# Optimization experiments

Hardware: AMD Instinct MI355X
Metric: run time of the kernel (lower is better)

Reference implementation:

```python
import jax, jax.numpy as jnp
import numpy as np

N_UNITS = 512
H = 8
D_K = N_UNITS // H  # 64
B = 4
T = 1024


def setup_inputs() -> dict:
    key = jax.random.key(0)
    ks = jax.random.split(key, 10)
    s = 0.02
    return {
        "x": jax.random.normal(ks[0], (B * T, N_UNITS), dtype=jnp.float32),
        "pos_k": jax.random.normal(ks[1], (T, T, D_K), dtype=jnp.float32),
        "batch_size": B,
        "Wq": jax.random.normal(ks[2], (N_UNITS, N_UNITS), dtype=jnp.float32) * s,
        "bq": jax.random.normal(ks[3], (N_UNITS,), dtype=jnp.float32) * s,
        "Wk": jax.random.normal(ks[4], (N_UNITS, N_UNITS), dtype=jnp.float32) * s,
        "bk": jax.random.normal(ks[5], (N_UNITS,), dtype=jnp.float32) * s,
        "Wv": jax.random.normal(ks[6], (N_UNITS, N_UNITS), dtype=jnp.float32) * s,
        "bv": jax.random.normal(ks[7], (N_UNITS,), dtype=jnp.float32) * s,
        "Wo": jax.random.normal(ks[8], (N_UNITS, N_UNITS), dtype=jnp.float32) * s,
        "bo": jax.random.normal(ks[9], (N_UNITS,), dtype=jnp.float32) * s,
    }


def reference(x, pos_k, batch_size, Wq, bq, Wk, bk, Wv, bv, Wo, bo):
    # x: [B*T, n_units]; pos_k: [T, T, d_k]
    q = (x @ Wq + bq).reshape(batch_size, -1, H, D_K).transpose(0, 2, 1, 3)  # [B,h,T,d]
    k = (x @ Wk + bk).reshape(batch_size, -1, H, D_K).transpose(0, 2, 1, 3)
    v = (x @ Wv + bv).reshape(batch_size, -1, H, D_K).transpose(0, 2, 1, 3)
    att_score = jnp.einsum("bhqd,bhkd->bhqk", q, k)
    # relative-position score: per query position t, q[:,:,t] @ pos_k[t].T
    att_score_pos = jnp.einsum("bhqd,qkd->bhqk", q, pos_k)
    scores = (att_score + att_score_pos) / np.sqrt(D_K).astype(np.float32)
    att = jax.nn.softmax(scores, axis=3)  # dropout p=0 -> identity (eval)
    out = jnp.einsum("bhqk,bhkd->bhqd", att, v)  # [B,h,T,d]
    out = out.transpose(0, 2, 1, 3).reshape(-1, H * D_K)  # [B*T, n_units]
    return out @ Wo + bo
```

## Files before the change

### kernel.cpp

```cpp
#include <hip/hip_runtime.h>


#define TT 1024
#define DH 64
#define NH 8
#define NU 512

typedef __bf16 bf16;
typedef bf16 bf16x8 __attribute__((ext_vector_type(8)));
typedef bf16 bf16x4 __attribute__((ext_vector_type(4)));
typedef float f32x4 __attribute__((ext_vector_type(4)));

#define MFMA16(a, b, c) __builtin_amdgcn_mfma_f32_16x16x32_bf16(a, b, c, 0, 0, 0)

__global__ __launch_bounds__(256) void cvtx_k(const float* __restrict__ x,
                                              bf16* __restrict__ xb) {
  int i = blockIdx.x * 256 + threadIdx.x;
  float4 v = ((const float4*)x)[i];
  bf16x4 o = {(bf16)v.x, (bf16)v.y, (bf16)v.z, (bf16)v.w};
  ((bf16x4*)xb)[i] = o;
}

__global__ __launch_bounds__(256) void wtrans_k(const float* __restrict__ Wq,
                                                const float* __restrict__ Wk,
                                                const float* __restrict__ Wv,
                                                const float* __restrict__ Wo,
                                                bf16* __restrict__ wt) {
  int n = blockIdx.x * 256 + threadIdx.x;
  int k0 = blockIdx.y * 8;
  int w = blockIdx.z;
  const float* W = (w == 0) ? Wq : (w == 1) ? Wk : (w == 2) ? Wv : Wo;
  bf16x8 v;
#pragma unroll
  for (int j = 0; j < 8; j++) v[j] = (bf16)W[(size_t)(k0 + j) * NU + n];
  *(bf16x8*)(wt + ((size_t)w * NU + n) * NU + k0) = v;
}

__global__ __launch_bounds__(256) void qkv_k(
    const bf16* __restrict__ xb, const bf16* __restrict__ wt,
    const float* __restrict__ bq, const float* __restrict__ bk,
    const float* __restrict__ bv, bf16* __restrict__ Qb, bf16* __restrict__ Kb,
    bf16* __restrict__ Vt) {
  int tid = threadIdx.x, wid = tid >> 6, ln = tid & 63;
  int n15 = ln & 15, qd = ln >> 4;
  int n0 = blockIdx.x * 64, m0 = blockIdx.y * 64;
  int mrow = m0 + wid * 16 + n15;

  const f32x4 fz = {0.f, 0.f, 0.f, 0.f};
  f32x4 acc[3][4];
#pragma unroll
  for (int w = 0; w < 3; w++)
#pragma unroll
    for (int nt = 0; nt < 4; nt++) acc[w][nt] = fz;

  for (int k0 = 0; k0 < NU; k0 += 32) {
    bf16x8 a = *(const bf16x8*)(xb + (size_t)mrow * NU + k0 + qd * 8);
#pragma unroll
    for (int w = 0; w < 3; w++)
#pragma unroll
      for (int nt = 0; nt < 4; nt++) {
        bf16x8 b = *(const bf16x8*)(wt + ((size_t)w * NU + n0 + nt * 16 + n15) * NU +
                                    k0 + qd * 8);
        acc[w][nt] = MFMA16(a, b, acc[w][nt]);
      }
  }

  int bb = m0 >> 10;
  int tbase = (m0 & 1023) + wid * 16 + qd * 4;
  int hh = n0 >> 6;
#pragma unroll
  for (int nt = 0; nt < 4; nt++) {
    int d = nt * 16 + n15;
    float bqv = bq[n0 + d], bkv = bk[n0 + d], bvv = bv[n0 + d];
    bf16x4 vv;
#pragma unroll
    for (int r = 0; r < 4; r++) {
      int t = tbase + r;
      size_t qk_idx = ((size_t)(bb * NH + hh) * TT + t) * DH + d;
      Qb[qk_idx] = (bf16)(acc[0][nt][r] + bqv);
      Kb[qk_idx] = (bf16)(acc[1][nt][r] + bkv);
      vv[r] = (bf16)(acc[2][nt][r] + bvv);
    }
    *(bf16x4*)(Vt + ((size_t)(bb * NH + hh) * DH + d) * TT + tbase) = vv;
  }
}

__global__ __launch_bounds__(256) void pos_gemm_k(const float* __restrict__ pos,
                                                  const bf16* __restrict__ Qb,
                                                  bf16* __restrict__ biasF) {
  int tid = threadIdx.x, wid = tid >> 6, ln = tid & 63;
  int n15 = ln & 15, qd = ln >> 4;
  int t = blockIdx.y;
  int s0b = blockIdx.x * 128;

  __shared__ bf16 Qs[32 * 72];
  {
    int bh = tid >> 3, dc = (tid & 7) * 8;
    *(bf16x8*)(&Qs[bh * 72 + dc]) =
        *(const bf16x8*)(Qb + ((size_t)bh * TT + t) * DH + dc);
  }
  __syncthreads();

  bf16x8 bQ[2][2];
#pragma unroll
  for (int bht = 0; bht < 2; bht++)
#pragma unroll
    for (int kc = 0; kc < 2; kc++)
      bQ[bht][kc] = *(const bf16x8*)(&Qs[(bht * 16 + n15) * 72 + kc * 32 + qd * 8]);

  const f32x4 fz = {0.f, 0.f, 0.f, 0.f};
  f32x4 acc[2][2];
#pragma unroll
  for (int stl = 0; stl < 2; stl++)
#pragma unroll
    for (int bht = 0; bht < 2; bht++) acc[stl][bht] = fz;

  int sw = s0b + wid * 32;
#pragma unroll
  for (int stl = 0; stl < 2; stl++) {
    const float* pr = pos + ((size_t)t * TT + sw + stl * 16 + n15) * DH + qd * 8;
#pragma unroll
    for (int kc = 0; kc < 2; kc++) {
      f32x4 u = __builtin_nontemporal_load((const f32x4*)(pr + kc * 32));
      f32x4 v = __builtin_nontemporal_load((const f32x4*)(pr + kc * 32 + 4));
      bf16x8 aP = {(bf16)u[0], (bf16)u[1], (bf16)u[2], (bf16)u[3],
                   (bf16)v[0], (bf16)v[1], (bf16)v[2], (bf16)v[3]};
#pragma unroll
      for (int bht = 0; bht < 2; bht++)
        acc[stl][bht] = MFMA16(aP, bQ[bht][kc], acc[stl][bht]);
    }
  }

  int t16 = t >> 4, tin = t & 15, s32 = (s0b >> 5) + wid;
#pragma unroll
  for (int bht = 0; bht < 2; bht++) {
    bf16x8 ov;
#pragma unroll
    for (int r = 0; r < 4; r++) {
      ov[r] = (bf16)acc[0][bht][r];
      ov[4 + r] = (bf16)acc[1][bht][r];
    }
    *(bf16x8*)(biasF +
               (((size_t)(bht * 16 + n15) * 64 + t16) * 32 + s32) * 512 +
               tin * 32 + qd * 8) = ov;
  }
}

__global__ __launch_bounds__(256) void flash_k(const bf16* __restrict__ Qb,
                                               const bf16* __restrict__ Kb,
                                               const bf16* __restrict__ Vt,
                                               const bf16* __restrict__ biasF,
                                               bf16* __restrict__ att) {
  int tid = threadIdx.x, wid = tid >> 6, ln = tid & 63;
  int n15 = ln & 15, qd = ln >> 4;
  int bh = blockIdx.x;
  int t0 = blockIdx.y * 64 + wid * 16;
  const float SC = 0.18033688f;

  __shared__ bf16 Pl[4][16][40];

  bf16x8 bQ[2];
#pragma unroll
  for (int kc = 0; kc < 2; kc++)
    bQ[kc] = *(const bf16x8*)(Qb + ((size_t)bh * TT + t0 + n15) * DH + kc * 32 + qd * 8);

  const bf16* Kbase = Kb + (size_t)bh * TT * DH;
  const bf16* Vbase = Vt + (size_t)bh * DH * TT;
  const bf16* Fbase = biasF + (((size_t)bh * 64 + (t0 >> 4)) * 32) * 512 +
                      n15 * 32 + qd * 8;

  const f32x4 fz = {0.f, 0.f, 0.f, 0.f};
  f32x4 accO[4] = {fz, fz, fz, fz};
  f32x4 accL = fz;
  const bf16 one = (bf16)1.0f;
  const bf16x8 onesv = {one, one, one, one, one, one, one, one};

  bf16x8 Kf[2][4], Vf[2][4];
  bf16x8 Bf[4];

  auto ldKV = [&](int buf, int s0) {
#pragma unroll
    for (int mt = 0; mt < 2; mt++)
#pragma unroll
      for (int kc = 0; kc < 2; kc++)
        Kf[buf][mt * 2 + kc] =
            *(const bf16x8*)(Kbase + (size_t)(s0 + mt * 16 + n15) * DH + kc * 32 + qd * 8);
#pragma unroll
    for (int dt = 0; dt < 4; dt++)
      Vf[buf][dt] = *(const bf16x8*)(Vbase + (size_t)(dt * 16 + n15) * TT + s0 + qd * 8);
  };
  auto ldB = [&](int buf, int s0) {
    Bf[buf] = *(const bf16x8*)(Fbase + (size_t)(s0 >> 5) * 512);
  };

  ldB(0, 0);
  ldB(1, 32);
  ldKV(0, 0);

#pragma unroll 4
  for (int it = 0; it < 32; it++) {
    int s0 = it * 32;
    ldKV((it + 1) & 1, (s0 + 32) & 1023);
    ldB((it + 2) & 3, (s0 + 64) & 1023);

    f32x4 accS[2] = {fz, fz};
#pragma unroll
    for (int mt = 0; mt < 2; mt++)
#pragma unroll
      for (int kc = 0; kc < 2; kc++)
        accS[mt] = MFMA16(Kf[it & 1][mt * 2 + kc], bQ[kc], accS[mt]);

#pragma unroll
    for (int mt = 0; mt < 2; mt++) {
      bf16x4 pb;
#pragma unroll
      for (int r = 0; r < 4; r++) {
        float p = __builtin_amdgcn_exp2f(
            (accS[mt][r] + (float)Bf[it & 3][mt * 4 + r]) * SC);
        pb[r] = (bf16)p;
      }
      *(bf16x4*)(&Pl[wid][n15][mt * 16 + qd * 4]) = pb;
    }
    bf16x8 bP = *(const bf16x8*)(&Pl[wid][n15][qd * 8]);
    accL = MFMA16(onesv, bP, accL);
#pragma unroll
    for (int dt = 0; dt < 4; dt++) accO[dt] = MFMA16(Vf[it & 1][dt], bP, accO[dt]);
  }

  int bb = bh >> 3, hh = bh & 7;
  float rcp = 1.0f / accL[0];
#pragma unroll
  for (int dt = 0; dt < 4; dt++) {
    bf16x4 ov;
#pragma unroll
    for (int r = 0; r < 4; r++) ov[r] = (bf16)(accO[dt][r] * rcp);
    *(bf16x4*)(att + ((size_t)bb * TT + t0 + n15) * NU + hh * DH + dt * 16 + qd * 4) = ov;
  }
}

__global__ __launch_bounds__(256) void proj_k(const bf16* __restrict__ att,
                                              const bf16* __restrict__ wt,
                                              const float* __restrict__ bo,
                                              float* __restrict__ out) {
  int tid = threadIdx.x, wid = tid >> 6, ln = tid & 63;
  int n15 = ln & 15, qd = ln >> 4;
  int n0 = blockIdx.x * 64, m0 = blockIdx.y * 64;
  int mrow = m0 + wid * 16 + n15;

  const f32x4 fz = {0.f, 0.f, 0.f, 0.f};
  f32x4 acc[4] = {fz, fz, fz, fz};
  for (int k0 = 0; k0 < NU; k0 += 32) {
    bf16x8 a = *(const bf16x8*)(att + (size_t)mrow * NU + k0 + qd * 8);
#pragma unroll
    for (int nt = 0; nt < 4; nt++) {
      bf16x8 b = *(const bf16x8*)(wt + ((size_t)3 * NU + n0 + nt * 16 + n15) * NU +
                                  k0 + qd * 8);
      acc[nt] = MFMA16(a, b, acc[nt]);
    }
  }
#pragma unroll
  for (int nt = 0; nt < 4; nt++) {
    int col = n0 + nt * 16 + n15;
    float bov = bo[col];
#pragma unroll
    for (int r = 0; r < 4; r++) {
      int row = m0 + wid * 16 + qd * 4 + r;
      out[(size_t)row * NU + col] = acc[nt][r] + bov;
    }
  }
}

extern "C" void kernel_launch(void* const* d_in, const int* in_sizes, int n_in,
                              void* d_out, int out_size, void* d_ws, size_t ws_size,
                              hipStream_t stream) {
  const float* x = (const float*)d_in[0];
  const float* pos = (const float*)d_in[1];
  const float* Wq = (const float*)d_in[3];
  const float* bq = (const float*)d_in[4];
  const float* Wk = (const float*)d_in[5];
  const float* bk = (const float*)d_in[6];
  const float* Wv = (const float*)d_in[7];
  const float* bv = (const float*)d_in[8];
  const float* Wo = (const float*)d_in[9];
  const float* bo = (const float*)d_in[10];
  float* out = (float*)d_out;

  char* ws = (char*)d_ws;
  bf16* xb = (bf16*)(ws);
  bf16* wt = (bf16*)(ws + ((size_t)4 << 20));
  bf16* Qb = (bf16*)(ws + ((size_t)6 << 20));
  bf16* Kb = (bf16*)(ws + ((size_t)10 << 20));
  bf16* Vt = (bf16*)(ws + ((size_t)14 << 20));
  bf16* att = (bf16*)(ws + ((size_t)18 << 20));
  bf16* biasF = (bf16*)(ws + ((size_t)22 << 20));

  cvtx_k<<<2048, 256, 0, stream>>>(x, xb);
  wtrans_k<<<dim3(2, 64, 4), 256, 0, stream>>>(Wq, Wk, Wv, Wo, wt);
  qkv_k<<<dim3(8, 64), 256, 0, stream>>>(xb, wt, bq, bk, bv, Qb, Kb, Vt);
  pos_gemm_k<<<dim3(8, 1024), 256, 0, stream>>>(pos, Qb, biasF);
  flash_k<<<dim3(32, 16), 256, 0, stream>>>(Qb, Kb, Vt, biasF, att);
  proj_k<<<dim3(8, 64), 256, 0, stream>>>(att, wt, bo, out);
}
```

Baseline: 527.7 us.

## Split attention over key halves, fuse prep kernels, narrow GEMM tiles

Merges the x conversion and weight transpose into one prep kernel, which saves a launch. The flash attention kernel is split into two key-range halves that write fp32 partial outputs and row sums, and a new combine kernel merges them into the bf16 attention output. This doubles the number of flash blocks so the GPU's compute units are better filled. The QKV and output projection GEMMs use 32-column tiles so they also launch twice as many blocks. In exchange there is extra global traffic for the fp32 partials, one extra launch, and less reuse of A loads in the GEMMs.

```diff
diff --git a/kernel.cpp b/kernel.cpp
--- a/kernel.cpp
+++ b/kernel.cpp
@@ -13,27 +13,31 @@
 
 #define MFMA16(a, b, c) __builtin_amdgcn_mfma_f32_16x16x32_bf16(a, b, c, 0, 0, 0)
 
-__global__ __launch_bounds__(256) void cvtx_k(const float* __restrict__ x,
-                                              bf16* __restrict__ xb) {
-  int i = blockIdx.x * 256 + threadIdx.x;
-  float4 v = ((const float4*)x)[i];
-  bf16x4 o = {(bf16)v.x, (bf16)v.y, (bf16)v.z, (bf16)v.w};
-  ((bf16x4*)xb)[i] = o;
-}
-
-__global__ __launch_bounds__(256) void wtrans_k(const float* __restrict__ Wq,
-                                                const float* __restrict__ Wk,
-                                                const float* __restrict__ Wv,
-                                                const float* __restrict__ Wo,
-                                                bf16* __restrict__ wt) {
-  int n = blockIdx.x * 256 + threadIdx.x;
-  int k0 = blockIdx.y * 8;
-  int w = blockIdx.z;
-  const float* W = (w == 0) ? Wq : (w == 1) ? Wk : (w == 2) ? Wv : Wo;
-  bf16x8 v;
-#pragma unroll
-  for (int j = 0; j < 8; j++) v[j] = (bf16)W[(size_t)(k0 + j) * NU + n];
-  *(bf16x8*)(wt + ((size_t)w * NU + n) * NU + k0) = v;
+__global__ __launch_bounds__(256) void prep_k(const float* __restrict__ x,
+                                              const float* __restrict__ Wq,
+                                              const float* __restrict__ Wk,
+                                              const float* __restrict__ Wv,
+                                              const float* __restrict__ Wo,
+                                              bf16* __restrict__ xb,
+                                              bf16* __restrict__ wt) {
+  int bid = blockIdx.x, tid = threadIdx.x;
+  {
+    int i = bid * 256 + tid;
+    float4 v = ((const float4*)x)[i];
+    bf16x4 o = {(bf16)v.x, (bf16)v.y, (bf16)v.z, (bf16)v.w};
+    ((bf16x4*)xb)[i] = o;
+  }
+  if ((bid & 3) == 0) {
+    int u = bid >> 2;
+    int w = u >> 7, rem = u & 127;
+    int k0 = (rem >> 1) * 8;
+    int n = (rem & 1) * 256 + tid;
+    const float* W = (w == 0) ? Wq : (w == 1) ? Wk : (w == 2) ? Wv : Wo;
+    bf16x8 v;
+#pragma unroll
+    for (int j = 0; j < 8; j++) v[j] = (bf16)W[(size_t)(k0 + j) * NU + n];
+    *(bf16x8*)(wt + ((size_t)w * NU + n) * NU + k0) = v;
+  }
 }
 
 __global__ __launch_bounds__(256) void qkv_k(
@@ -43,22 +47,22 @@
     bf16* __restrict__ Vt) {
   int tid = threadIdx.x, wid = tid >> 6, ln = tid & 63;
   int n15 = ln & 15, qd = ln >> 4;
-  int n0 = blockIdx.x * 64, m0 = blockIdx.y * 64;
+  int n0 = blockIdx.x * 32, m0 = blockIdx.y * 64;
   int mrow = m0 + wid * 16 + n15;
 
   const f32x4 fz = {0.f, 0.f, 0.f, 0.f};
-  f32x4 acc[3][4];
+  f32x4 acc[3][2];
 #pragma unroll
   for (int w = 0; w < 3; w++)
 #pragma unroll
-    for (int nt = 0; nt < 4; nt++) acc[w][nt] = fz;
+    for (int nt = 0; nt < 2; nt++) acc[w][nt] = fz;
 
   for (int k0 = 0; k0 < NU; k0 += 32) {
     bf16x8 a = *(const bf16x8*)(xb + (size_t)mrow * NU + k0 + qd * 8);
 #pragma unroll
     for (int w = 0; w < 3; w++)
 #pragma unroll
-      for (int nt = 0; nt < 4; nt++) {
+      for (int nt = 0; nt < 2; nt++) {
         bf16x8 b = *(const bf16x8*)(wt + ((size_t)w * NU + n0 + nt * 16 + n15) * NU +
                                     k0 + qd * 8);
         acc[w][nt] = MFMA16(a, b, acc[w][nt]);
@@ -69,9 +73,10 @@
   int tbase = (m0 & 1023) + wid * 16 + qd * 4;
   int hh = n0 >> 6;
 #pragma unroll
-  for (int nt = 0; nt < 4; nt++) {
-    int d = nt * 16 + n15;
-    float bqv = bq[n0 + d], bkv = bk[n0 + d], bvv = bv[n0 + d];
+  for (int nt = 0; nt < 2; nt++) {
+    int col = n0 + nt * 16 + n15;
+    int d = (n0 & 63) + nt * 16 + n15;
+    float bqv = bq[col], bkv = bk[col], bvv = bv[col];
     bf16x4 vv;
 #pragma unroll
     for (int r = 0; r < 4; r++) {
@@ -146,15 +151,18 @@
   }
 }
 
-__global__ __launch_bounds__(256) void flash_k(const bf16* __restrict__ Qb,
-                                               const bf16* __restrict__ Kb,
-                                               const bf16* __restrict__ Vt,
-                                               const bf16* __restrict__ biasF,
-                                               bf16* __restrict__ att) {
+__global__ __launch_bounds__(256) void flash_part_k(const bf16* __restrict__ Qb,
+                                                    const bf16* __restrict__ Kb,
+                                                    const bf16* __restrict__ Vt,
+                                                    const bf16* __restrict__ biasF,
+                                                    float* __restrict__ partO,
+                                                    float* __restrict__ partL) {
   int tid = threadIdx.x, wid = tid >> 6, ln = tid & 63;
   int n15 = ln & 15, qd = ln >> 4;
   int bh = blockIdx.x;
   int t0 = blockIdx.y * 64 + wid * 16;
+  int sh = blockIdx.z;
+  int sB = sh * 512;
   const float SC = 0.18033688f;
 
   __shared__ bf16 Pl[4][16][40];
@@ -193,15 +201,15 @@
     Bf[buf] = *(const bf16x8*)(Fbase + (size_t)(s0 >> 5) * 512);
   };
 
-  ldB(0, 0);
-  ldB(1, 32);
-  ldKV(0, 0);
+  ldB(0, sB);
+  ldB(1, sB + 32);
+  ldKV(0, sB);
 
 #pragma unroll 4
-  for (int it = 0; it < 32; it++) {
-    int s0 = it * 32;
-    ldKV((it + 1) & 1, (s0 + 32) & 1023);
-    ldB((it + 2) & 3, (s0 + 64) & 1023);
+  for (int it = 0; it < 16; it++) {
+    int s0 = sB + it * 32;
+    ldKV((it + 1) & 1, sB + (((it + 1) * 32) & 511));
+    ldB((it + 2) & 3, sB + (((it + 2) * 32) & 511));
 
     f32x4 accS[2] = {fz, fz};
 #pragma unroll
@@ -227,14 +235,31 @@
     for (int dt = 0; dt < 4; dt++) accO[dt] = MFMA16(Vf[it & 1][dt], bP, accO[dt]);
   }
 
+  int t = t0 + n15;
+  float* po = partO + (((size_t)sh * 32 + bh) * TT + t) * DH + qd * 4;
+#pragma unroll
+  for (int dt = 0; dt < 4; dt++) *(f32x4*)(po + dt * 16) = accO[dt];
+  if (qd == 0) partL[((size_t)sh * 32 + bh) * TT + t] = accL[0];
+}
+
+__global__ __launch_bounds__(256) void combine_k(const float* __restrict__ partO,
+                                                 const float* __restrict__ partL,
+                                                 bf16* __restrict__ att) {
+  int idx = blockIdx.x * 256 + threadIdx.x;
+  int bh = idx >> 10, t = idx & 1023;
+  const float* pa = partO + ((size_t)bh * TT + t) * DH;
+  const float* pb = partO + (((size_t)32 + bh) * TT + t) * DH;
+  float rcp = 1.0f / (partL[(size_t)bh * TT + t] + partL[((size_t)32 + bh) * TT + t]);
   int bb = bh >> 3, hh = bh & 7;
-  float rcp = 1.0f / accL[0];
-#pragma unroll
-  for (int dt = 0; dt < 4; dt++) {
+  bf16* ao = att + ((size_t)bb * TT + t) * NU + hh * DH;
+#pragma unroll
+  for (int j = 0; j < 16; j++) {
+    f32x4 a = *(const f32x4*)(pa + j * 4);
+    f32x4 b = *(const f32x4*)(pb + j * 4);
     bf16x4 ov;
 #pragma unroll
-    for (int r = 0; r < 4; r++) ov[r] = (bf16)(accO[dt][r] * rcp);
-    *(bf16x4*)(att + ((size_t)bb * TT + t0 + n15) * NU + hh * DH + dt * 16 + qd * 4) = ov;
+    for (int r = 0; r < 4; r++) ov[r] = (bf16)((a[r] + b[r]) * rcp);
+    *(bf16x4*)(ao + j * 4) = ov;
   }
 }
 
@@ -244,22 +269,22 @@
                                               float* __restrict__ out) {
   int tid = threadIdx.x, wid = tid >> 6, ln = tid & 63;
   int n15 = ln & 15, qd = ln >> 4;
-  int n0 = blockIdx.x * 64, m0 = blockIdx.y * 64;
+  int n0 = blockIdx.x * 32, m0 = blockIdx.y * 64;
   int mrow = m0 + wid * 16 + n15;
 
   const f32x4 fz = {0.f, 0.f, 0.f, 0.f};
-  f32x4 acc[4] = {fz, fz, fz, fz};
+  f32x4 acc[2] = {fz, fz};
   for (int k0 = 0; k0 < NU; k0 += 32) {
     bf16x8 a = *(const bf16x8*)(att + (size_t)mrow * NU + k0 + qd * 8);
 #pragma unroll
-    for (int nt = 0; nt < 4; nt++) {
+    for (int nt = 0; nt < 2; nt++) {
       bf16x8 b = *(const bf16x8*)(wt + ((size_t)3 * NU + n0 + nt * 16 + n15) * NU +
                                   k0 + qd * 8);
       acc[nt] = MFMA16(a, b, acc[nt]);
     }
   }
 #pragma unroll
-  for (int nt = 0; nt < 4; nt++) {
+  for (int nt = 0; nt < 2; nt++) {
     int col = n0 + nt * 16 + n15;
     float bov = bo[col];
 #pragma unroll
@@ -293,11 +318,13 @@
   bf16* Vt = (bf16*)(ws + ((size_t)14 << 20));
   bf16* att = (bf16*)(ws + ((size_t)18 << 20));
   bf16* biasF = (bf16*)(ws + ((size_t)22 << 20));
-
-  cvtx_k<<<2048, 256, 0, stream>>>(x, xb);
-  wtrans_k<<<dim3(2, 64, 4), 256, 0, stream>>>(Wq, Wk, Wv, Wo, wt);
-  qkv_k<<<dim3(8, 64), 256, 0, stream>>>(xb, wt, bq, bk, bv, Qb, Kb, Vt);
+  float* partO = (float*)(ws + ((size_t)88 << 20));
+  float* partL = (float*)(ws + ((size_t)106 << 20));
+
+  prep_k<<<2048, 256, 0, stream>>>(x, Wq, Wk, Wv, Wo, xb, wt);
+  qkv_k<<<dim3(16, 64), 256, 0, stream>>>(xb, wt, bq, bk, bv, Qb, Kb, Vt);
   pos_gemm_k<<<dim3(8, 1024), 256, 0, stream>>>(pos, Qb, biasF);
-  flash_k<<<dim3(32, 16), 256, 0, stream>>>(Qb, Kb, Vt, biasF, att);
-  proj_k<<<dim3(8, 64), 256, 0, stream>>>(att, wt, bo, out);
-}
+  flash_part_k<<<dim3(32, 16, 2), 256, 0, stream>>>(Qb, Kb, Vt, biasF, partO, partL);
+  combine_k<<<128, 256, 0, stream>>>(partO, partL, att);
+  proj_k<<<dim3(16, 64), 256, 0, stream>>>(att, wt, bo, out);
+}
```

After: 534.4 us. About the same (+1.3%).
